# Kernel optimization log

Hardware: AMD Instinct MI355X
Metric: run time of the kernel (lower is better)

Reference implementation:

```python
import jax, jax.numpy as jnp
import numpy as np

E, H, I = 16, 2048, 768
B, S = 4, 1024
TOPK = 8
BLK_R, BLK_C = 128, 128


def blockwise_dequantize(w, scale_inv, r, c):
    # w: [E, M, N] (fp8 values stored as fp32 here), scale_inv: [E, M//r, N//c]
    e, m, n = w.shape
    wb = w.reshape(e, m // r, r, n // c, c)
    wb = wb * scale_inv[:, :, None, :, None]
    return wb.reshape(e, m, n)


def setup_inputs() -> dict:
    key = jax.random.key(0)
    ks = jax.random.split(key, 7)
    return {
        "hidden_states": jax.random.normal(ks[0], (B, S, H), dtype=jnp.float32),
        "routing_weights": jax.random.uniform(ks[1], (B * S, E), dtype=jnp.float32),
        "gate_up_proj": jax.random.normal(ks[2], (E, H, 2 * I), dtype=jnp.float32),
        "gate_up_proj_scale_inv": jax.random.uniform(ks[3], (E, H // BLK_R, 2 * I // BLK_C), dtype=jnp.float32),
        "down_proj": jax.random.normal(ks[4], (E, I, H), dtype=jnp.float32),
        "down_proj_scale_inv": jax.random.uniform(ks[5], (E, I // BLK_R, H // BLK_C), dtype=jnp.float32),
        "router_indices": jax.random.randint(ks[6], (B * S, TOPK), 0, E, dtype=jnp.int64 if jax.config.jax_enable_x64 else jnp.int32),
    }


def reference(hidden_states, routing_weights, gate_up_proj, gate_up_proj_scale_inv,
              down_proj, down_proj_scale_inv, router_indices):
    batch_size = hidden_states.shape[0]
    hs = hidden_states.reshape(-1, H)                      # [T, H], T = B*S
    x = jnp.broadcast_to(hs[None], (E,) + hs.shape)        # repeat across experts

    gu_w = blockwise_dequantize(gate_up_proj, gate_up_proj_scale_inv, BLK_R, BLK_C)   # [E, H, 2I]
    dn_w = blockwise_dequantize(down_proj, down_proj_scale_inv, BLK_R, BLK_C)         # [E, I, H]

    gate_up = jnp.einsum('eth,ehf->etf', x, gu_w)          # [E, T, 2I]
    gate, up = jnp.split(gate_up, 2, axis=-1)
    inter = up * jax.nn.silu(gate)                         # [E, T, I]
    next_states = jnp.einsum('eti,eih->eth', inter, dn_w)  # [E, T, H]

    next_states = next_states.reshape(E, batch_size, -1, H)
    rw = routing_weights.T.reshape(E, batch_size, -1)      # [E, B, S]
    out = (next_states * rw[..., None]).sum(axis=0)        # [B, S, H]
    return out
```

## Files before the change

### kernel.cpp

```cpp
#include <hip/hip_runtime.h>
#include <hip/hip_bf16.h>
#include <cstdint>

#define E_     16
#define H_     2048
#define I_     768
#define T_     4096
#define TWO_I  1536
#define K2_    (E_ * I_)

typedef __bf16 bf16x8 __attribute__((ext_vector_type(8)));
typedef float  floatx4 __attribute__((ext_vector_type(4)));

__device__ __forceinline__ void gload_lds16(const void* g, void* l) {
  __builtin_amdgcn_global_load_lds(
      (const __attribute__((address_space(1))) void*)(void*)g,
      (__attribute__((address_space(3))) void*)l,
      16, 0, 0);
}

#define ASM_VMCNT(n) asm volatile("s_waitcnt vmcnt(" #n ")" ::: "memory")
#define ASM_LGKM0()  asm volatile("s_waitcnt lgkmcnt(0)" ::: "memory")
#define SBAR()       __builtin_amdgcn_s_barrier()
#define SCHED0()     __builtin_amdgcn_sched_barrier(0)

__global__ void k_convert(const float* __restrict__ in, __bf16* __restrict__ out) {
  size_t idx = ((size_t)blockIdx.x * blockDim.x + threadIdx.x) * 8;
  float4 a = *(const float4*)(in + idx);
  float4 b = *(const float4*)(in + idx + 4);
  bf16x8 o;
  o[0] = (__bf16)a.x; o[1] = (__bf16)a.y; o[2] = (__bf16)a.z; o[3] = (__bf16)a.w;
  o[4] = (__bf16)b.x; o[5] = (__bf16)b.y; o[6] = (__bf16)b.z; o[7] = (__bf16)b.w;
  *(bf16x8*)(out + idx) = o;
}

__global__ void k_dq_transpose(const float* __restrict__ src, __bf16* __restrict__ dst,
                               const float* __restrict__ scale, int R, int C,
                               size_t slab, size_t rowStride, int ilvHalf) {
  const int e  = blockIdx.z;
  const int n0 = blockIdx.x * 64;
  const int m0 = blockIdx.y * 64;
  __shared__ float tile[64 * 65];
  const float s = scale[((size_t)e * (R >> 7) + (m0 >> 7)) * (C >> 7) + (n0 >> 7)];
  const float* sp = src + ((size_t)e * R + m0) * C + n0;
  const int t  = threadIdx.x;
  const int c4 = (t & 15) * 4;
  const int rb = t >> 4;
  #pragma unroll
  for (int p = 0; p < 4; ++p) {
    int r = p * 16 + rb;
    float4 v = *(const float4*)(sp + (size_t)r * C + c4);
    tile[(c4 + 0) * 65 + r] = v.x * s;
    tile[(c4 + 1) * 65 + r] = v.y * s;
    tile[(c4 + 2) * 65 + r] = v.z * s;
    tile[(c4 + 3) * 65 + r] = v.w * s;
  }
  __syncthreads();
  const int c8 = (t & 7) * 8;
  const int r0 = t >> 3;
  #pragma unroll
  for (int p = 0; p < 2; ++p) {
    int nr = r0 + p * 32;
    int ng = n0 + nr;
    int np;
    if (ilvHalf) {
      int h = (ng >= ilvHalf) ? 1 : 0;
      int iLoc = ng - h * ilvHalf;
      np = ((iLoc >> 5) << 6) + h * 32 + (iLoc & 31);
    } else {
      np = ng;
    }
    const float* row = &tile[nr * 65 + c8];
    bf16x8 o;
    #pragma unroll
    for (int j = 0; j < 8; ++j) o[j] = (__bf16)row[j];
    *(bf16x8*)(dst + (size_t)e * slab + (size_t)np * rowStride + m0 + c8) = o;
  }
}

#define STG_A(tt, h) do { int b_ = ((tt)&1)*16384 + (h)*8192; \
    gload_lds16(aSrc + (size_t)((h)*128)*LDK + (tt)*64, dA + b_); \
    gload_lds16(aSrc + (size_t)((h)*128 + 64)*LDK + (tt)*64, dA + b_ + 4096); } while (0)
#define STG_B(tt, h) do { int b_ = ((tt)&1)*16384 + (h)*8192; \
    gload_lds16(bSrc + (size_t)((h)*128)*LDK + (tt)*64, dB + b_); \
    gload_lds16(bSrc + (size_t)((h)*128 + 64)*LDK + (tt)*64, dB + b_ + 4096); } while (0)

#define AF4(MI0) do { \
    af[0][0] = *(const bf16x8*)(pA + (MI0)*1024 + kc0); \
    af[0][1] = *(const bf16x8*)(pA + (MI0)*1024 + kc1); \
    af[1][0] = *(const bf16x8*)(pA + ((MI0)+1)*1024 + kc0); \
    af[1][1] = *(const bf16x8*)(pA + ((MI0)+1)*1024 + kc1); } while (0)

#define MFMA16(MI0) do { \
    _Pragma("unroll") \
    for (int ii = 0; ii < 2; ++ii) { \
      _Pragma("unroll") \
      for (int ni = 0; ni < 4; ++ni) { \
        acc[(MI0)+ii][ni] = __builtin_amdgcn_mfma_f32_16x16x32_bf16(af[ii][0], bb[ni][0], acc[(MI0)+ii][ni], 0, 0, 0); \
        acc[(MI0)+ii][ni] = __builtin_amdgcn_mfma_f32_16x16x32_bf16(af[ii][1], bb[ni][1], acc[(MI0)+ii][ni], 0, 0, 0); \
      } \
    } } while (0)

#define PHASE(MI0, STAGE_STMT, CKPT_STMT) do { \
    AF4(MI0); \
    STAGE_STMT; \
    CKPT_STMT; \
    SBAR(); \
    ASM_LGKM0(); \
    SCHED0(); \
    __builtin_amdgcn_s_setprio(1); \
    MFMA16(MI0); \
    __builtin_amdgcn_s_setprio(0); \
    SBAR(); \
  } while (0)

__global__ __launch_bounds__(512, 2)
void k_gemm1(const __bf16* __restrict__ A, const __bf16* __restrict__ W,
             const float* __restrict__ rw, __bf16* __restrict__ inter) {
  extern __shared__ __align__(16) __bf16 smem[];
  __bf16* sA = smem;
  __bf16* sB = smem + 32768;
  float*  sRW = (float*)(smem + 65536);

  const int lid = blockIdx.x + 16 * (blockIdx.y + 6 * blockIdx.z);
  const int nid = (lid & 7) * 192 + (lid >> 3);
  const int e  = nid / 96;
  const int r_ = nid - e * 96;
  const int by = r_ >> 4;
  const int m0 = (r_ & 15) * 256;
  const int n0 = by * 256;

  const int t    = threadIdx.x;
  const int wave = t >> 6, lane = t & 63;
  const int wm = wave >> 2, wn = wave & 3;
  const int l4 = lane >> 4, r16 = lane & 15;
  const int LDK = H_;

  if (t < 256) sRW[t] = rw[(size_t)(m0 + t) * E_ + e];
  ASM_VMCNT(0);

  const int rowSt = t >> 3;
  const int kcSt  = ((t & 7) ^ ((t >> 3) & 7)) << 3;
  const __bf16* aSrc = A + (size_t)(m0 + rowSt) * H_ + kcSt;
  const __bf16* bSrc = W + ((size_t)e * TWO_I + n0 + rowSt) * H_ + kcSt;
  __bf16* dA = sA + wave * 512;
  __bf16* dB = sB + wave * 512;

  const int kc0 = (l4 ^ (r16 & 7)) << 3;
  const int kc1 = ((4 + l4) ^ (r16 & 7)) << 3;
  const __bf16* pArd = sA + wm * 8192 + r16 * 64;
  const __bf16* pBrd = sB + (wn >> 1) * 8192 + ((wn & 1) * 64 + r16) * 64;

  floatx4 acc[8][4];
  #pragma unroll
  for (int mi = 0; mi < 8; ++mi)
    #pragma unroll
    for (int ni = 0; ni < 4; ++ni) {
      floatx4 z = {0.f, 0.f, 0.f, 0.f};
      acc[mi][ni] = z;
    }

  STG_B(0, 0); STG_B(0, 1); STG_A(0, 0); STG_A(0, 1);
  STG_B(1, 0); STG_B(1, 1);
  ASM_VMCNT(4);
  SBAR();

  const int NT = H_ / 64;
  for (int tt = 0; tt < NT; ++tt) {
    const int bo = (tt & 1) * 16384;
    const __bf16* pA = pArd + bo;
    const __bf16* pB = pBrd + bo;
    bf16x8 bb[4][2], af[2][2];
    #pragma unroll
    for (int ni = 0; ni < 4; ++ni) {
      bb[ni][0] = *(const bf16x8*)(pB + ni * 1024 + kc0);
      bb[ni][1] = *(const bf16x8*)(pB + ni * 1024 + kc1);
    }
    PHASE(0, if (tt + 1 < NT) STG_A(tt + 1, 0), (void)0);
    PHASE(2, if (tt + 1 < NT) STG_A(tt + 1, 1), (void)0);
    PHASE(4, if (tt + 2 < NT) STG_B(tt + 2, 0), (void)0);
    PHASE(6, if (tt + 2 < NT) STG_B(tt + 2, 1),
             if (tt + 2 < NT) { ASM_VMCNT(4); } else { ASM_VMCNT(0); });
  }

  const int rq = l4 * 4;
  const int gBase = (by * 4 + wn) * 32;
  #pragma unroll
  for (int mi = 0; mi < 8; ++mi) {
    const int rl = wm * 128 + mi * 16 + rq;
    #pragma unroll
    for (int ni = 0; ni < 2; ++ni) {
      const size_t colIdx = (size_t)e * I_ + gBase + ni * 16 + r16;
      #pragma unroll
      for (int r = 0; r < 4; ++r) {
        float g = acc[mi][ni][r];
        float u = acc[mi][ni + 2][r];
        float sil = g / (1.0f + __expf(-g));
        float val = u * sil * sRW[rl + r];
        inter[(size_t)(m0 + rl + r) * K2_ + colIdx] = (__bf16)val;
      }
    }
  }
}

__global__ __launch_bounds__(512, 2)
void k_gemm2(const __bf16* __restrict__ Ainter, const __bf16* __restrict__ W,
             float* __restrict__ out0, float* __restrict__ out1) {
  extern __shared__ __align__(16) __bf16 smem[];
  __bf16* sA = smem;
  __bf16* sB = smem + 32768;

  const int lid = blockIdx.x + 16 * (blockIdx.y + 8 * blockIdx.z);
  const int nid = (lid & 7) * 32 + (lid >> 3);
  const int bz = nid >> 7;
  const int r_ = nid & 127;
  const int n0 = (r_ >> 4) * 256;
  const int m0 = (r_ & 15) * 256;
  float* dst = bz ? out1 : out0;
  const size_t kOff = (size_t)bz * (K2_ / 2);

  const int t    = threadIdx.x;
  const int wave = t >> 6, lane = t & 63;
  const int wm = wave >> 2, wn = wave & 3;
  const int l4 = lane >> 4, r16 = lane & 15;
  const int LDK = K2_;

  const int rowSt = t >> 3;
  const int kcSt  = ((t & 7) ^ ((t >> 3) & 7)) << 3;
  const __bf16* aSrc = Ainter + (size_t)(m0 + rowSt) * K2_ + kOff + kcSt;
  const __bf16* bSrc = W      + (size_t)(n0 + rowSt) * K2_ + kOff + kcSt;
  __bf16* dA = sA + wave * 512;
  __bf16* dB = sB + wave * 512;

  const int kc0 = (l4 ^ (r16 & 7)) << 3;
  const int kc1 = ((4 + l4) ^ (r16 & 7)) << 3;
  const __bf16* pArd = sA + wm * 8192 + r16 * 64;
  const __bf16* pBrd = sB + (wn >> 1) * 8192 + ((wn & 1) * 64 + r16) * 64;

  floatx4 acc[8][4];
  #pragma unroll
  for (int mi = 0; mi < 8; ++mi)
    #pragma unroll
    for (int ni = 0; ni < 4; ++ni) {
      floatx4 z = {0.f, 0.f, 0.f, 0.f};
      acc[mi][ni] = z;
    }

  STG_B(0, 0); STG_B(0, 1); STG_A(0, 0); STG_A(0, 1);
  STG_B(1, 0); STG_B(1, 1);
  ASM_VMCNT(4);
  SBAR();

  const int NT = (K2_ / 2) / 64;
  for (int tt = 0; tt < NT; ++tt) {
    const int bo = (tt & 1) * 16384;
    const __bf16* pA = pArd + bo;
    const __bf16* pB = pBrd + bo;
    bf16x8 bb[4][2], af[2][2];
    #pragma unroll
    for (int ni = 0; ni < 4; ++ni) {
      bb[ni][0] = *(const bf16x8*)(pB + ni * 1024 + kc0);
      bb[ni][1] = *(const bf16x8*)(pB + ni * 1024 + kc1);
    }
    PHASE(0, if (tt + 1 < NT) STG_A(tt + 1, 0), (void)0);
    PHASE(2, if (tt + 1 < NT) STG_A(tt + 1, 1), (void)0);
    PHASE(4, if (tt + 2 < NT) STG_B(tt + 2, 0), (void)0);
    PHASE(6, if (tt + 2 < NT) STG_B(tt + 2, 1),
             if (tt + 2 < NT) { ASM_VMCNT(4); } else { ASM_VMCNT(0); });
  }

  const int rq = l4 * 4;
  #pragma unroll
  for (int mi = 0; mi < 8; ++mi) {
    const int rl = wm * 128 + mi * 16 + rq;
    #pragma unroll
    for (int ni = 0; ni < 4; ++ni) {
      const int cl = wn * 64 + ni * 16 + r16;
      #pragma unroll
      for (int r = 0; r < 4; ++r)
        dst[(size_t)(m0 + rl + r) * H_ + n0 + cl] = acc[mi][ni][r];
    }
  }
}

__global__ void k_addout(float* __restrict__ out, const float* __restrict__ part) {
  size_t i = ((size_t)blockIdx.x * blockDim.x + threadIdx.x) * 4;
  float4 a = *(const float4*)(out + i);
  float4 b = *(const float4*)(part + i);
  a.x += b.x; a.y += b.y; a.z += b.z; a.w += b.w;
  *(float4*)(out + i) = a;
}

extern "C" void kernel_launch(void* const* d_in, const int* in_sizes, int n_in,
                              void* d_out, int out_size, void* d_ws, size_t ws_size,
                              hipStream_t stream) {
  const float* hs   = (const float*)d_in[0];
  const float* rw   = (const float*)d_in[1];
  const float* gup  = (const float*)d_in[2];
  const float* gups = (const float*)d_in[3];
  const float* dnp  = (const float*)d_in[4];
  const float* dnps = (const float*)d_in[5];
  float* out = (float*)d_out;

  char* ws = (char*)d_ws;
  __bf16* hsb  = (__bf16*)ws;
  __bf16* wgu  = (__bf16*)(ws + (size_t)(16 << 20));
  __bf16* wdn  = (__bf16*)(ws + (size_t)(112 << 20));
  __bf16* intr = (__bf16*)(ws + (size_t)(160 << 20));
  float* part = (float*)(ws + (size_t)(16 << 20));

  static int inited = 0;
  if (!inited) {
    hipFuncSetAttribute((const void*)k_gemm1,
                        hipFuncAttributeMaxDynamicSharedMemorySize, 132096);
    hipFuncSetAttribute((const void*)k_gemm2,
                        hipFuncAttributeMaxDynamicSharedMemorySize, 131072);
    inited = 1;
  }

  k_convert<<<(T_ * H_) / (256 * 8), 256, 0, stream>>>(hs, hsb);
  k_dq_transpose<<<dim3(TWO_I / 64, H_ / 64, E_), 256, 0, stream>>>(
      gup, wgu, gups, H_, TWO_I, (size_t)TWO_I * H_, (size_t)H_, I_);
  k_dq_transpose<<<dim3(H_ / 64, I_ / 64, E_), 256, 0, stream>>>(
      dnp, wdn, dnps, I_, H_, (size_t)I_, (size_t)K2_, 0);
  k_gemm1<<<dim3(T_ / 256, TWO_I / 256, E_), 512, 132096, stream>>>(hsb, wgu, rw, intr);
  k_gemm2<<<dim3(T_ / 256, H_ / 256, 2), 512, 131072, stream>>>(intr, wdn, out, part);
  k_addout<<<(T_ * H_) / (256 * 4), 256, 0, stream>>>(out, part);
}
```

Baseline: 920.3 us.

## Merge prep kernels and double-buffer A-fragment LDS reads in GEMM loops

Merges the activation conversion and the two weight dequant-transpose kernels into one launch, which removes two kernel launches and the tail gaps between them. In both GEMMs, A fragments now ping-pong between two register sets, so the LDS read for the next phase is issued before the current MFMA batch, and the lgkmcnt waits are relaxed to allow overlap. The prologue now waits for all initial loads, and the last K tile is peeled into its own body. This costs extra VGPRs, which under launch_bounds(512,2) could cause spills.

```diff
diff --git a/kernel.cpp b/kernel.cpp
--- a/kernel.cpp
+++ b/kernel.cpp
@@ -20,27 +20,18 @@
 }
 
 #define ASM_VMCNT(n) asm volatile("s_waitcnt vmcnt(" #n ")" ::: "memory")
-#define ASM_LGKM0()  asm volatile("s_waitcnt lgkmcnt(0)" ::: "memory")
+#define ASM_LGKM(n)  asm volatile("s_waitcnt lgkmcnt(" #n ")" ::: "memory")
 #define SBAR()       __builtin_amdgcn_s_barrier()
 #define SCHED0()     __builtin_amdgcn_sched_barrier(0)
-
-__global__ void k_convert(const float* __restrict__ in, __bf16* __restrict__ out) {
-  size_t idx = ((size_t)blockIdx.x * blockDim.x + threadIdx.x) * 8;
-  float4 a = *(const float4*)(in + idx);
-  float4 b = *(const float4*)(in + idx + 4);
-  bf16x8 o;
-  o[0] = (__bf16)a.x; o[1] = (__bf16)a.y; o[2] = (__bf16)a.z; o[3] = (__bf16)a.w;
-  o[4] = (__bf16)b.x; o[5] = (__bf16)b.y; o[6] = (__bf16)b.z; o[7] = (__bf16)b.w;
-  *(bf16x8*)(out + idx) = o;
-}
-
-__global__ void k_dq_transpose(const float* __restrict__ src, __bf16* __restrict__ dst,
-                               const float* __restrict__ scale, int R, int C,
-                               size_t slab, size_t rowStride, int ilvHalf) {
-  const int e  = blockIdx.z;
-  const int n0 = blockIdx.x * 64;
-  const int m0 = blockIdx.y * 64;
-  __shared__ float tile[64 * 65];
+#define PRIO1()      __builtin_amdgcn_s_setprio(1)
+#define PRIO0()      __builtin_amdgcn_s_setprio(0)
+
+__device__ __forceinline__ void dq_body(const float* __restrict__ src,
+                                        __bf16* __restrict__ dst,
+                                        const float* __restrict__ scale,
+                                        int e, int n0, int m0, int R, int C,
+                                        size_t slab, size_t rowStride, int ilvHalf,
+                                        float* tile) {
   const float s = scale[((size_t)e * (R >> 7) + (m0 >> 7)) * (C >> 7) + (n0 >> 7)];
   const float* sp = src + ((size_t)e * R + m0) * C + n0;
   const int t  = threadIdx.x;
@@ -78,6 +69,40 @@
   }
 }
 
+__global__ void k_prep(const float* __restrict__ hs, __bf16* __restrict__ hsb,
+                       const float* __restrict__ gup, __bf16* __restrict__ wgu,
+                       const float* __restrict__ gups,
+                       const float* __restrict__ dnp, __bf16* __restrict__ wdn,
+                       const float* __restrict__ dnps) {
+  __shared__ float tile[64 * 65];
+  const int id = blockIdx.x;
+  if (id < 4096) {
+    size_t idx = ((size_t)id * blockDim.x + threadIdx.x) * 8;
+    float4 a = *(const float4*)(hs + idx);
+    float4 b = *(const float4*)(hs + idx + 4);
+    bf16x8 o;
+    o[0] = (__bf16)a.x; o[1] = (__bf16)a.y; o[2] = (__bf16)a.z; o[3] = (__bf16)a.w;
+    o[4] = (__bf16)b.x; o[5] = (__bf16)b.y; o[6] = (__bf16)b.z; o[7] = (__bf16)b.w;
+    *(bf16x8*)(hsb + idx) = o;
+  } else if (id < 4096 + 12288) {
+    const int id2 = id - 4096;
+    const int bx = id2 % 24;
+    const int rest = id2 / 24;
+    const int by = rest & 31;
+    const int e  = rest >> 5;
+    dq_body(gup, wgu, gups, e, bx * 64, by * 64, H_, TWO_I,
+            (size_t)TWO_I * H_, (size_t)H_, I_, tile);
+  } else {
+    const int id3 = id - (4096 + 12288);
+    const int bx = id3 & 31;
+    const int rest = id3 >> 5;
+    const int by = rest % 12;
+    const int e  = rest / 12;
+    dq_body(dnp, wdn, dnps, e, bx * 64, by * 64, I_, H_,
+            (size_t)I_, (size_t)K2_, 0, tile);
+  }
+}
+
 #define STG_A(tt, h) do { int b_ = ((tt)&1)*16384 + (h)*8192; \
     gload_lds16(aSrc + (size_t)((h)*128)*LDK + (tt)*64, dA + b_); \
     gload_lds16(aSrc + (size_t)((h)*128 + 64)*LDK + (tt)*64, dA + b_ + 4096); } while (0)
@@ -85,33 +110,76 @@
     gload_lds16(bSrc + (size_t)((h)*128)*LDK + (tt)*64, dB + b_); \
     gload_lds16(bSrc + (size_t)((h)*128 + 64)*LDK + (tt)*64, dB + b_ + 4096); } while (0)
 
-#define AF4(MI0) do { \
-    af[0][0] = *(const bf16x8*)(pA + (MI0)*1024 + kc0); \
-    af[0][1] = *(const bf16x8*)(pA + (MI0)*1024 + kc1); \
-    af[1][0] = *(const bf16x8*)(pA + ((MI0)+1)*1024 + kc0); \
-    af[1][1] = *(const bf16x8*)(pA + ((MI0)+1)*1024 + kc1); } while (0)
-
-#define MFMA16(MI0) do { \
+#define AFLD(DST, MI0) do { \
+    DST[0][0] = *(const bf16x8*)(pA + (MI0)*1024 + kc0); \
+    DST[0][1] = *(const bf16x8*)(pA + (MI0)*1024 + kc1); \
+    DST[1][0] = *(const bf16x8*)(pA + ((MI0)+1)*1024 + kc0); \
+    DST[1][1] = *(const bf16x8*)(pA + ((MI0)+1)*1024 + kc1); } while (0)
+
+#define BBLD() do { \
+    _Pragma("unroll") \
+    for (int ni = 0; ni < 4; ++ni) { \
+      bb[ni][0] = *(const bf16x8*)(pB + ni * 1024 + kc0); \
+      bb[ni][1] = *(const bf16x8*)(pB + ni * 1024 + kc1); \
+    } } while (0)
+
+#define MFMA16(MI0, AF) do { \
     _Pragma("unroll") \
     for (int ii = 0; ii < 2; ++ii) { \
       _Pragma("unroll") \
       for (int ni = 0; ni < 4; ++ni) { \
-        acc[(MI0)+ii][ni] = __builtin_amdgcn_mfma_f32_16x16x32_bf16(af[ii][0], bb[ni][0], acc[(MI0)+ii][ni], 0, 0, 0); \
-        acc[(MI0)+ii][ni] = __builtin_amdgcn_mfma_f32_16x16x32_bf16(af[ii][1], bb[ni][1], acc[(MI0)+ii][ni], 0, 0, 0); \
+        acc[(MI0)+ii][ni] = __builtin_amdgcn_mfma_f32_16x16x32_bf16(AF[ii][0], bb[ni][0], acc[(MI0)+ii][ni], 0, 0, 0); \
+        acc[(MI0)+ii][ni] = __builtin_amdgcn_mfma_f32_16x16x32_bf16(AF[ii][1], bb[ni][1], acc[(MI0)+ii][ni], 0, 0, 0); \
       } \
     } } while (0)
 
-#define PHASE(MI0, STAGE_STMT, CKPT_STMT) do { \
-    AF4(MI0); \
-    STAGE_STMT; \
-    CKPT_STMT; \
-    SBAR(); \
-    ASM_LGKM0(); \
-    SCHED0(); \
-    __builtin_amdgcn_s_setprio(1); \
-    MFMA16(MI0); \
-    __builtin_amdgcn_s_setprio(0); \
-    SBAR(); \
+#define TILE_BODY_STAGED(tt, NT) do { \
+    const int bo = ((tt) & 1) * 16384; \
+    const __bf16* pA = pArd + bo; \
+    const __bf16* pB = pBrd + bo; \
+    bf16x8 bb[4][2], afA[2][2], afB[2][2]; \
+    BBLD(); \
+    AFLD(afA, 0); \
+     \
+    AFLD(afB, 2); \
+    STG_A((tt) + 1, 0); \
+    SBAR(); ASM_LGKM(4); SCHED0(); \
+    PRIO1(); MFMA16(0, afA); PRIO0(); SBAR(); \
+     \
+    AFLD(afA, 4); \
+    STG_A((tt) + 1, 1); \
+    SBAR(); ASM_LGKM(4); SCHED0(); \
+    PRIO1(); MFMA16(2, afB); PRIO0(); SBAR(); \
+     \
+    AFLD(afB, 6); \
+    if ((tt) + 2 < (NT)) STG_B((tt) + 2, 0); \
+    SBAR(); ASM_LGKM(4); SCHED0(); \
+    PRIO1(); MFMA16(4, afA); PRIO0(); SBAR(); \
+     \
+    if ((tt) + 2 < (NT)) { STG_B((tt) + 2, 1); ASM_VMCNT(4); } \
+    else                 { ASM_VMCNT(0); } \
+    SBAR(); ASM_LGKM(0); SCHED0(); \
+    PRIO1(); MFMA16(6, afB); PRIO0(); SBAR(); \
+  } while (0)
+
+#define TILE_BODY_LAST(tt) do { \
+    const int bo = ((tt) & 1) * 16384; \
+    const __bf16* pA = pArd + bo; \
+    const __bf16* pB = pBrd + bo; \
+    bf16x8 bb[4][2], afA[2][2], afB[2][2]; \
+    BBLD(); \
+    AFLD(afA, 0); \
+    AFLD(afB, 2); \
+    SBAR(); ASM_LGKM(4); SCHED0(); \
+    PRIO1(); MFMA16(0, afA); PRIO0(); SBAR(); \
+    AFLD(afA, 4); \
+    SBAR(); ASM_LGKM(4); SCHED0(); \
+    PRIO1(); MFMA16(2, afB); PRIO0(); SBAR(); \
+    AFLD(afB, 6); \
+    SBAR(); ASM_LGKM(4); SCHED0(); \
+    PRIO1(); MFMA16(4, afA); PRIO0(); SBAR(); \
+    SBAR(); ASM_LGKM(0); SCHED0(); \
+    PRIO1(); MFMA16(6, afB); PRIO0(); SBAR(); \
   } while (0)
 
 __global__ __launch_bounds__(512, 2)
@@ -137,7 +205,6 @@
   const int LDK = H_;
 
   if (t < 256) sRW[t] = rw[(size_t)(m0 + t) * E_ + e];
-  ASM_VMCNT(0);
 
   const int rowSt = t >> 3;
   const int kcSt  = ((t & 7) ^ ((t >> 3) & 7)) << 3;
@@ -162,26 +229,14 @@
 
   STG_B(0, 0); STG_B(0, 1); STG_A(0, 0); STG_A(0, 1);
   STG_B(1, 0); STG_B(1, 1);
-  ASM_VMCNT(4);
+  ASM_VMCNT(0);
   SBAR();
 
   const int NT = H_ / 64;
-  for (int tt = 0; tt < NT; ++tt) {
-    const int bo = (tt & 1) * 16384;
-    const __bf16* pA = pArd + bo;
-    const __bf16* pB = pBrd + bo;
-    bf16x8 bb[4][2], af[2][2];
-    #pragma unroll
-    for (int ni = 0; ni < 4; ++ni) {
-      bb[ni][0] = *(const bf16x8*)(pB + ni * 1024 + kc0);
-      bb[ni][1] = *(const bf16x8*)(pB + ni * 1024 + kc1);
-    }
-    PHASE(0, if (tt + 1 < NT) STG_A(tt + 1, 0), (void)0);
-    PHASE(2, if (tt + 1 < NT) STG_A(tt + 1, 1), (void)0);
-    PHASE(4, if (tt + 2 < NT) STG_B(tt + 2, 0), (void)0);
-    PHASE(6, if (tt + 2 < NT) STG_B(tt + 2, 1),
-             if (tt + 2 < NT) { ASM_VMCNT(4); } else { ASM_VMCNT(0); });
-  }
+  for (int tt = 0; tt < NT - 1; ++tt) {
+    TILE_BODY_STAGED(tt, NT);
+  }
+  TILE_BODY_LAST(NT - 1);
 
   const int rq = l4 * 4;
   const int gBase = (by * 4 + wn) * 32;
@@ -248,26 +303,14 @@
 
   STG_B(0, 0); STG_B(0, 1); STG_A(0, 0); STG_A(0, 1);
   STG_B(1, 0); STG_B(1, 1);
-  ASM_VMCNT(4);
+  ASM_VMCNT(0);
   SBAR();
 
   const int NT = (K2_ / 2) / 64;
-  for (int tt = 0; tt < NT; ++tt) {
-    const int bo = (tt & 1) * 16384;
-    const __bf16* pA = pArd + bo;
-    const __bf16* pB = pBrd + bo;
-    bf16x8 bb[4][2], af[2][2];
-    #pragma unroll
-    for (int ni = 0; ni < 4; ++ni) {
-      bb[ni][0] = *(const bf16x8*)(pB + ni * 1024 + kc0);
-      bb[ni][1] = *(const bf16x8*)(pB + ni * 1024 + kc1);
-    }
-    PHASE(0, if (tt + 1 < NT) STG_A(tt + 1, 0), (void)0);
-    PHASE(2, if (tt + 1 < NT) STG_A(tt + 1, 1), (void)0);
-    PHASE(4, if (tt + 2 < NT) STG_B(tt + 2, 0), (void)0);
-    PHASE(6, if (tt + 2 < NT) STG_B(tt + 2, 1),
-             if (tt + 2 < NT) { ASM_VMCNT(4); } else { ASM_VMCNT(0); });
-  }
+  for (int tt = 0; tt < NT - 1; ++tt) {
+    TILE_BODY_STAGED(tt, NT);
+  }
+  TILE_BODY_LAST(NT - 1);
 
   const int rq = l4 * 4;
   #pragma unroll
@@ -318,11 +361,8 @@
     inited = 1;
   }
 
-  k_convert<<<(T_ * H_) / (256 * 8), 256, 0, stream>>>(hs, hsb);
-  k_dq_transpose<<<dim3(TWO_I / 64, H_ / 64, E_), 256, 0, stream>>>(
-      gup, wgu, gups, H_, TWO_I, (size_t)TWO_I * H_, (size_t)H_, I_);
-  k_dq_transpose<<<dim3(H_ / 64, I_ / 64, E_), 256, 0, stream>>>(
-      dnp, wdn, dnps, I_, H_, (size_t)I_, (size_t)K2_, 0);
+  k_prep<<<4096 + 12288 + 6144, 256, 0, stream>>>(hs, hsb, gup, wgu, gups,
+                                                  dnp, wdn, dnps);
   k_gemm1<<<dim3(T_ / 256, TWO_I / 256, E_), 512, 132096, stream>>>(hsb, wgu, rw, intr);
   k_gemm2<<<dim3(T_ / 256, H_ / 256, 2), 512, 131072, stream>>>(intr, wdn, out, part);
   k_addout<<<(T_ * H_) / (256 * 4), 256, 0, stream>>>(out, part);
```

Result: no change. 918.7 us (-0.2%).
